# Optimization experiments

Measured on AMD Instinct MI355X. Metric: run time of the kernel, lower is better.

Reference implementation:

```python
import math
import jax, jax.numpy as jnp
import numpy as np

B, L, DM = 2, 1024, 1024
STATE, EXPAND, CONV, DTR = 16, 2, 4, 8
INNER = DM * EXPAND          # 2048
NFFT = L // 2 + 1            # 513


def _silu(v):
    return v * jax.nn.sigmoid(v)


def setup_inputs() -> dict:
    key = jax.random.key(0)
    ks = jax.random.split(key, 12)
    s = lambda k, shape, sc=0.02: (jax.random.normal(k, shape, jnp.float32) * sc)
    # dt_proj bias initialized like the torch module: exp(U(0,1)*(log dt_max - log dt_min) + log dt_min)
    inv_dt = jnp.exp(jax.random.uniform(ks[10], (INNER,), jnp.float32)
                     * (math.log(0.1) - math.log(0.001)) + math.log(0.001))
    return {
        "x": jax.random.normal(ks[0], (B, L, DM), jnp.float32),
        "in_proj_w": s(ks[1], (2 * INNER, DM)),
        "conv_w": s(ks[2], (INNER, 1, CONV), 0.1),      # depthwise conv kernel
        "conv_b": jnp.zeros((INNER,), jnp.float32),
        "A_log": jnp.tile(jnp.log(jnp.arange(1, STATE + 1, dtype=jnp.float32)), (INNER, 1)),
        "D": jnp.ones((INNER,), jnp.float32),
        "x_proj_w": s(ks[3], (DTR + 2 * STATE, INNER)),
        "dt_proj_w": s(ks[4], (INNER, DTR)),
        "dt_proj_b": inv_dt,
        "filter_real": s(ks[5], (INNER, NFFT)),
        "filter_imag": s(ks[6], (INNER, NFFT)),
        "spectral_decay": jnp.ones((INNER,), jnp.float32) * 0.01,
        "fusion_w": s(ks[7], (INNER, 2 * INNER)),
        "fusion_b": jnp.zeros((INNER,), jnp.float32),
        "out_proj_w": s(ks[8], (DM, INNER)),
        "ln_gamma": jnp.ones((DM,), jnp.float32),
        "ln_beta": jnp.zeros((DM,), jnp.float32),
    }


def reference(x, in_proj_w, conv_w, conv_b, A_log, D, x_proj_w, dt_proj_w, dt_proj_b,
              filter_real, filter_imag, spectral_decay, fusion_w, fusion_b,
              out_proj_w, ln_gamma, ln_beta):
    residual = x
    xz = x @ in_proj_w.T                                   # [B,L,2*INNER]
    x_inner, z = xz[..., :INNER], xz[..., INNER:]
    z = _silu(z)

    # ---- SSM path ----
    xc = jnp.swapaxes(x_inner, 1, 2)                       # [B,E,L]
    xc = jax.lax.conv_general_dilated(
        xc, conv_w, (1,), [(CONV - 1, 0)],                 # causal depthwise conv (pad-left == torch pad + truncate)
        dimension_numbers=("NCH", "OIH", "NCH"),
        feature_group_count=INNER) + conv_b[None, :, None]
    x_conv = jnp.swapaxes(_silu(xc), 1, 2)                 # [B,L,E]

    x_dbc = x_conv @ x_proj_w.T                            # [B,L,DTR+2S]
    dt_x = x_dbc[..., :DTR]
    Bm = x_dbc[..., DTR:DTR + STATE]                       # [B,L,S]
    Cm = x_dbc[..., DTR + STATE:]                          # [B,L,S]
    dt = jax.nn.softplus(dt_x @ dt_proj_w.T + dt_proj_b)   # [B,L,E]
    A = -jnp.exp(A_log)                                    # [E,S]
    dA = jnp.exp(dt[..., None] * A)                        # [B,L,E,S]
    dBx = (dt * x_conv)[..., None] * Bm[:, :, None, :]     # [B,L,E,S]

    def step(h, inp):
        dA_t, dBx_t, C_t = inp
        h = dA_t * h + dBx_t                               # [B,E,S]
        return h, jnp.einsum('bes,bs->be', h, C_t)

    h0 = jnp.zeros((B, INNER, STATE), x.dtype)
    _, ys = jax.lax.scan(step, h0,
                         (jnp.swapaxes(dA, 0, 1), jnp.swapaxes(dBx, 0, 1), jnp.swapaxes(Cm, 0, 1)))
    y_ssm = jnp.swapaxes(ys, 0, 1) + x_conv * D            # [B,L,E]

    # ---- Spectral path ----
    xf = jnp.fft.rfft(jnp.swapaxes(x_inner, 1, 2), axis=-1)        # [B,E,NFFT]
    freqs = jnp.linspace(0.0, 1.0, NFFT)
    filt = (filter_real + 1j * filter_imag) * jnp.exp(-spectral_decay[:, None] * freqs[None, :])
    y_spec = jnp.swapaxes(jnp.fft.irfft(xf * filt[None], n=L, axis=-1), 1, 2)  # [B,L,E]

    # ---- Gated fusion ----
    g = jax.nn.sigmoid(jnp.concatenate([y_ssm, y_spec], -1) @ fusion_w.T + fusion_b)
    y = g * y_ssm + (1.0 - g) * y_spec
    y = y * z
    out = y @ out_proj_w.T + residual                      # [B,L,DM]

    mu = out.mean(-1, keepdims=True)
    var = out.var(-1, keepdims=True)
    return (out - mu) / jnp.sqrt(var + 1e-5) * ln_gamma + ln_beta
```

## Files before the change

### kernel.cpp

```cpp
#include <hip/hip_runtime.h>
#include <math.h>

#define B_ 2
#define L_ 1024
#define DM_ 1024
#define STATE_ 16
#define CONV_ 4
#define DTR_ 8
#define INNER_ 2048
#define M_ (B_*L_)
#define MD_ (B_*INNER_)
#define NFFT_ 513
#define NFP_ 1088
#define NCH_ 32
#define CHL_ 32
#define SK_ 16
#define KSL_ (2048/SK_)

typedef unsigned short u16;
typedef __attribute__((ext_vector_type(8))) short short8;
typedef __attribute__((ext_vector_type(8))) __bf16 bf16x8;
typedef __attribute__((ext_vector_type(4))) float f32x4;

__device__ __forceinline__ float frcp_(float x) { return __builtin_amdgcn_rcpf(x); }
__device__ __forceinline__ float fexp_(float x) { return __expf(x); }
__device__ __forceinline__ float fsigm_(float x) { return frcp_(1.f + __expf(-x)); }
__device__ __forceinline__ float fsilu_(float x) { return x * frcp_(1.f + __expf(-x)); }
__device__ __forceinline__ float fsoftplus_(float v) {
  return (v > 20.f) ? v : __logf(1.f + __expf(v));
}
__device__ __forceinline__ u16 f2bf(float f) {
  union { float f; unsigned u; } v; v.f = f;
  unsigned r = v.u + 0x7fffu + ((v.u >> 16) & 1u);
  return (u16)(r >> 16);
}
__device__ __forceinline__ float bf2f(u16 h) {
  union { unsigned u; float f; } v; v.u = ((unsigned)h) << 16;
  return v.f;
}
__device__ __forceinline__ void gload16(const void* g, void* l) {
  __builtin_amdgcn_global_load_lds(
      (const __attribute__((address_space(1))) unsigned*)g,
      (__attribute__((address_space(3))) unsigned*)l, 16, 0, 0);
}
__device__ __forceinline__ f32x4 mfma_bf16(short8 a, short8 b, f32x4 c) {
  return __builtin_amdgcn_mfma_f32_16x16x32_bf16(
      __builtin_bit_cast(bf16x8, a), __builtin_bit_cast(bf16x8, b), c, 0, 0, 0);
}

#define CVT2_N0 2097152
#define CVT2_NT 6291456
__global__ __launch_bounds__(256) void cvt2_k(
    const float* __restrict__ s0, const float* __restrict__ s1,
    u16* __restrict__ out)
{
  int i = (blockIdx.x*256 + threadIdx.x) * 4;
  const float* src; int off;
  if (i < CVT2_N0) { src = s0; off = 0; }
  else             { src = s1; off = CVT2_N0; }
  float4 v = *(const float4*)(src + (i - off));
  ushort4 o;
  o.x = f2bf(v.x); o.y = f2bf(v.y); o.z = f2bf(v.z); o.w = f2bf(v.w);
  *(ushort4*)(out + i) = o;
}

__device__ __forceinline__ void cvt16_body(int eb, int nthr, int t,
    const float* __restrict__ src, u16* __restrict__ dst)
{
  int i = (eb*nthr + t)*16;
  #pragma unroll
  for (int q = 0; q < 4; q++) {
    float4 v = *(const float4*)(src + i + q*4);
    ushort4 o;
    o.x = f2bf(v.x); o.y = f2bf(v.y); o.z = f2bf(v.z); o.w = f2bf(v.w);
    *(ushort4*)(dst + i + q*4) = o;
  }
}

__device__ __forceinline__ void conv_body(int idx, const float* __restrict__ xz,
    const float* __restrict__ cw, const float* __restrict__ cb,
    float* __restrict__ xc)
{
  int c = idx & (INNER_-1);
  int g = idx >> 11;
  int b = g >> 7;
  int lb = (g & 127) * 8;
  float w0=cw[c*4+0], w1=cw[c*4+1], w2=cw[c*4+2], w3=cw[c*4+3];
  float bias = cb[c];
  float v[11];
  #pragma unroll
  for (int j = 0; j < 11; j++) {
    int l = lb - 3 + j;
    v[j] = (l >= 0) ? xz[((size_t)((b << 10) + l))*4096 + c] : 0.f;
  }
  #pragma unroll
  for (int j = 0; j < 8; j++) {
    float s = bias + w0*v[j] + w1*v[j+1] + w2*v[j+2] + w3*v[j+3];
    xc[((size_t)((b << 10) + lb + j))*INNER_ + c] = fsilu_(s);
  }
}

__device__ __forceinline__ void genWdft_body(int idx, u16* __restrict__ W)
{
  int l = idx & (L_-1);
  int col = idx >> 10;
  float v = 0.f;
  int f = col >> 1;
  if (f < NFFT_) {
    int ph = (l*f) & (L_-1);
    float th = (float)ph * (6.283185307179586f / (float)L_);
    v = (col & 1) ? -__sinf(th) : __cosf(th);
  }
  W[idx] = f2bf(v);
}

__device__ __forceinline__ void genWinv_body(int idx, u16* __restrict__ W)
{
  int r = idx % NFP_;
  int l = idx / NFP_;
  int f = r >> 1;
  float v = 0.f;
  if (f < NFFT_) {
    bool edge = (f == 0) || (f == 512);
    float sc = (edge ? 1.f : 2.f) / (float)L_;
    int ph = (f*l) & (L_-1);
    float th = (float)ph * (6.283185307179586f / (float)L_);
    if (r & 1) v = edge ? 0.f : -sc*__sinf(th);
    else       v = sc*__cosf(th);
  }
  W[idx] = f2bf(v);
}

__device__ __forceinline__ void xproj_body(int eb,
    const float* __restrict__ xconv, const float* __restrict__ W,
    float* __restrict__ part, void* lds)
{
  float (*Bs)[KSL_+4] = (float(*)[KSL_+4])lds;
  const int sk = eb & (SK_-1), mt = eb / SK_;
  const int k0 = sk*KSL_;
  for (int i = threadIdx.x; i < 40*KSL_; i += 256) {
    int n = i / KSL_, k = i & (KSL_-1);
    Bs[n][k] = W[(size_t)n*2048 + k0 + k];
  }
  __syncthreads();
  const int m = mt*256 + threadIdx.x;
  const float* arow = xconv + (size_t)m*2048 + k0;
  float acc[40];
  #pragma unroll
  for (int j=0;j<40;j++) acc[j]=0.f;
  for (int k = 0; k < KSL_; k += 4) {
    float4 a = *(const float4*)(arow + k);
    #pragma unroll
    for (int j = 0; j < 40; j++) {
      float4 b = *(const float4*)&Bs[j][k];
      acc[j] += a.x*b.x + a.y*b.y + a.z*b.z + a.w*b.w;
    }
  }
  float* o = part + ((size_t)sk*M_ + m)*40;
  #pragma unroll
  for (int j = 0; j < 10; j++)
    *(float4*)(o + j*4) = make_float4(acc[j*4], acc[j*4+1], acc[j*4+2], acc[j*4+3]);
}

template<int TM, int TN, int EPI, int YCH, int AUX, int KS>
__global__ __launch_bounds__((TM/64)*(TN/32)*64) void mgemm_k(
    const u16* __restrict__ Ab, const u16* __restrict__ Bb,
    void* __restrict__ Cout, int K, int ldc,
    const float* __restrict__ aux0, u16* __restrict__ aux1,
    const float* __restrict__ aux2, const float* __restrict__ aux3,
    int gx, int gy,
    const float* __restrict__ ga, const float* __restrict__ gb,
    const float* __restrict__ gc, float* __restrict__ go,
    u16* __restrict__ gw,
    int ldk, const float* __restrict__ cvs, u16* __restrict__ cvd)
{
  constexpr int WN   = TN/32;
  constexpr int NW   = (TM/64)*WN;
  constexpr int NTHR = NW*64;
  __shared__ __align__(16) u16 As[2][TM*64];
  __shared__ __align__(16) u16 Bs[2][TN*64];
  const int t = threadIdx.x;
  const int nwg = gx * gy;

  if constexpr (AUX != 0) {
    int eb = (int)blockIdx.x - nwg*KS;
    if (eb >= 0) {
      if constexpr (AUX == 1) {
        if (eb < 2176) genWdft_body(eb*NTHR + t, gw);
        else           cvt16_body(eb - 2176, NTHR, t, cvs, cvd);
      } else if constexpr (AUX == 2) {
        if (eb < 2048)      conv_body(eb*256 + t, ga, gb, gc, go);
        else if (eb < 6400) genWinv_body((eb - 2048)*256 + t, gw);
        else                cvt16_body(eb - 6400, NTHR, t, cvs, cvd);
      } else {
        xproj_body(eb, ga, gb, go, (void*)&As[0][0]);
      }
      return;
    }
  }

  const int lane = t & 63;
  const int w = t >> 6;
  const int wm = w / WN, wn = w % WN;

  int bid = blockIdx.x;
  int ks = 0;
  if constexpr (KS > 1) { ks = bid / nwg; bid -= ks*nwg; }
  const int k0 = ks * K;
  const int lid = (bid & 7) * (nwg >> 3) + (bid >> 3);
  int bx, by;
  if (YCH) { by = lid / gx; bx = lid - by*gx; }
  else     { bx = lid / gy; by = lid - bx*gy; }
  const int M0 = by * TM, N0 = bx * TN;

  f32x4 acc[4][2] = {};

  auto stage = [&](int buf, int kk0) {
    #pragma unroll
    for (int q = 0; q < TM*8/NTHR; q++) {
      int u = q*NTHR + t;
      int row = u >> 3, gpr = u & 7;
      int grp = gpr ^ (row & 7);
      gload16(Ab + (size_t)(M0+row)*ldk + k0 + kk0 + grp*8, &As[buf][u*8]);
    }
    #pragma unroll
    for (int q = 0; q < TN*8/NTHR; q++) {
      int u = q*NTHR + t;
      int row = u >> 3, gpr = u & 7;
      int grp = gpr ^ (row & 7);
      gload16(Bb + (size_t)(N0+row)*ldk + k0 + kk0 + grp*8, &Bs[buf][u*8]);
    }
  };

  stage(0, 0);
  const int nk = K >> 6;
  for (int kst = 0; kst < nk; kst++) {
    const int buf = kst & 1;
    __syncthreads();
    if (kst + 1 < nk) stage(buf ^ 1, (kst + 1) << 6);
    const u16* Asb = As[buf];
    const u16* Bsb = Bs[buf];
    #pragma unroll
    for (int kk = 0; kk < 2; kk++) {
      const int quad = lane >> 4;
      const int grp = kk*4 + quad;
      short8 af[4], bfr[2];
      #pragma unroll
      for (int i = 0; i < 4; i++) {
        int row = wm*64 + i*16 + (lane & 15);
        af[i] = *(const short8*)&Asb[(row*8 + (grp ^ (row & 7)))*8];
      }
      #pragma unroll
      for (int j = 0; j < 2; j++) {
        int row = wn*32 + j*16 + (lane & 15);
        bfr[j] = *(const short8*)&Bsb[(row*8 + (grp ^ (row & 7)))*8];
      }
      #pragma unroll
      for (int i = 0; i < 4; i++)
        #pragma unroll
        for (int j = 0; j < 2; j++)
          acc[i][j] = mfma_bf16(af[i], bfr[j], acc[i][j]);
    }
  }

  #pragma unroll
  for (int i = 0; i < 4; i++) {
    int mbase = M0 + wm*64 + i*16 + (lane >> 4)*4;
    #pragma unroll
    for (int j = 0; j < 2; j++) {
      int n = N0 + wn*32 + j*16 + (lane & 15);
      #pragma unroll
      for (int r = 0; r < 4; r++) {
        int m = mbase + r;
        float v = acc[i][j][r];
        if (EPI == 0) {
          ((float*)Cout)[(size_t)m*ldc + n] = v;
        } else if (EPI == 3) {
          float pv = __shfl_xor(v, 1, 64);
          int f = n >> 1;
          float outv = 0.f;
          if (f < NFFT_) {
            int c = m & (INNER_-1);
            float d  = fexp_(-aux2[c] * (float)f * (1.f/512.f));
            float wr = aux0[c*NFFT_+f]*d, wi = aux3[c*NFFT_+f]*d;
            float a = (n & 1) ? pv : v;
            float b = (n & 1) ? v : pv;
            outv = (n & 1) ? (a*wi + b*wr) : (a*wr - b*wi);
          }
          ((u16*)Cout)[(size_t)m*ldc + n] = f2bf(outv);
        } else if (EPI == 5) {
          ((float*)Cout)[(size_t)m*ldc + n] = v;
          if (n < 2048) {
            int b2 = m >> 10, l2 = m & 1023;
            aux1[((size_t)(b2*2048 + n) << 10) + l2] = f2bf(v);
          }
        } else if (EPI == 6) {
          int b2 = m >> 11, c2 = m & (INNER_-1);
          ((u16*)Cout)[((size_t)((b2 << 10) + n) << 12) + 2048 + c2] = f2bf(v);
        } else {
          float* P = (float*)Cout + (size_t)ks * ((size_t)gy*TM*ldc);
          P[(size_t)m*ldc + n] = v;
        }
      }
    }
  }
}

__global__ __launch_bounds__(256) void combine_gate_k(
    const float* __restrict__ P, const float* __restrict__ fus_b,
    const u16* __restrict__ ycat, const float* __restrict__ xz,
    u16* __restrict__ ycomb)
{
  int i4 = (blockIdx.x*256 + threadIdx.x)*4;
  int m = i4 >> 11, n = i4 & 2047;
  float4 p0 = *(const float4*)(P + i4);
  float4 p1 = *(const float4*)(P + 4194304 + i4);
  ushort4 ysv = *(const ushort4*)(ycat + (size_t)m*4096 + n);
  ushort4 ypv = *(const ushort4*)(ycat + (size_t)m*4096 + 2048 + n);
  float4 zv = *(const float4*)(xz + (size_t)m*4096 + 2048 + n);
  float4 fb = *(const float4*)(fus_b + n);
  float pp[4] = {p0.x+p1.x, p0.y+p1.y, p0.z+p1.z, p0.w+p1.w};
  float zz[4] = {zv.x, zv.y, zv.z, zv.w};
  float bb[4] = {fb.x, fb.y, fb.z, fb.w};
  u16 ys[4] = {ysv.x, ysv.y, ysv.z, ysv.w};
  u16 yp[4] = {ypv.x, ypv.y, ypv.z, ypv.w};
  ushort4 o;
  u16* op = (u16*)&o;
  #pragma unroll
  for (int j = 0; j < 4; j++) {
    float g = fsigm_(pp[j] + bb[j]);
    op[j] = f2bf((g*bf2f(ys[j]) + (1.f-g)*bf2f(yp[j]))*fsilu_(zz[j]));
  }
  *(ushort4*)(ycomb + i4) = o;
}

__global__ __launch_bounds__(256) void xpred_k(const float* __restrict__ part,
                                               float* __restrict__ xdbc)
{
  int i = blockIdx.x*256 + threadIdx.x;
  float s = 0.f;
  #pragma unroll
  for (int sk = 0; sk < SK_; sk++) s += part[(size_t)sk*81920 + i];
  xdbc[i] = s;
}

__global__ __launch_bounds__(256) void scan1_k(
    const float* __restrict__ xdbc, const float* __restrict__ xconv,
    const float* __restrict__ A_log, const float* __restrict__ dtw,
    const float* __restrict__ dtb, float* __restrict__ Pq)
{
  int idx = blockIdx.x*256 + threadIdx.x;
  int e  = idx & (INNER_-1);
  int bc = idx >> 11;
  int ch = bc & (NCH_-1);
  int b  = bc >> 5;
  float A[STATE_];
  #pragma unroll
  for (int s=0;s<STATE_;s++) A[s] = -fexp_(A_log[e*STATE_+s]);
  float w[DTR_];
  #pragma unroll
  for (int r=0;r<DTR_;r++) w[r] = dtw[e*DTR_+r];
  float bias = dtb[e];
  float h[STATE_] = {};
  float sdt = 0.f;
  int mbase = b*L_ + ch*CHL_;
  float dtx[DTR_], Bv[STATE_], xcv;
  {
    const float* row = xdbc + (size_t)mbase*40;
    #pragma unroll
    for (int r=0;r<DTR_;r++) dtx[r] = row[r];
    #pragma unroll
    for (int s=0;s<STATE_;s++) Bv[s] = row[8+s];
    xcv = xconv[(size_t)mbase*INNER_ + e];
  }
  for (int l=0;l<CHL_;l++) {
    float ndtx[DTR_], nBv[STATE_], nxcv = 0.f;
    if (l+1 < CHL_) {
      const float* nrow = xdbc + (size_t)(mbase+l+1)*40;
      #pragma unroll
      for (int r=0;r<DTR_;r++) ndtx[r] = nrow[r];
      #pragma unroll
      for (int s=0;s<STATE_;s++) nBv[s] = nrow[8+s];
      nxcv = xconv[(size_t)(mbase+l+1)*INNER_ + e];
    } else {
      #pragma unroll
      for (int r=0;r<DTR_;r++) ndtx[r] = 0.f;
      #pragma unroll
      for (int s=0;s<STATE_;s++) nBv[s] = 0.f;
    }
    float v = bias;
    #pragma unroll
    for (int r=0;r<DTR_;r++) v += dtx[r]*w[r];
    float dt = fsoftplus_(v);
    sdt += dt;
    float dx = dt * xcv;
    #pragma unroll
    for (int s=0;s<STATE_;s++) {
      float dA = fexp_(dt*A[s]);
      h[s] = dA*h[s] + dx*Bv[s];
    }
    #pragma unroll
    for (int r=0;r<DTR_;r++) dtx[r] = ndtx[r];
    #pragma unroll
    for (int s=0;s<STATE_;s++) Bv[s] = nBv[s];
    xcv = nxcv;
  }
  float* o = Pq + (size_t)idx*32;
  #pragma unroll
  for (int s=0;s<STATE_;s++) { o[s] = fexp_(A[s]*sdt); o[16+s] = h[s]; }
}

__global__ __launch_bounds__(256) void scan2_k(float* __restrict__ Pq)
{
  int idx = blockIdx.x*256 + threadIdx.x;
  int s = idx & 15;
  int e = (idx >> 4) & (INNER_-1);
  int b = idx >> 15;
  float h = 0.f;
  for (int ch = 0; ch < NCH_; ch++) {
    size_t base = ((size_t)(b*NCH_+ch)*INNER_ + e)*32;
    float p = Pq[base + s];
    float q = Pq[base + 16 + s];
    Pq[base + 16 + s] = h;
    h = p*h + q;
  }
}

__global__ __launch_bounds__(256) void scan3_k(
    const float* __restrict__ xdbc, const float* __restrict__ xconv,
    const float* __restrict__ A_log, const float* __restrict__ dtw,
    const float* __restrict__ dtb, const float* __restrict__ Dp,
    const float* __restrict__ Pq, u16* __restrict__ ycat)
{
  int idx = blockIdx.x*256 + threadIdx.x;
  int e  = idx & (INNER_-1);
  int bc = idx >> 11;
  int ch = bc & (NCH_-1);
  int b  = bc >> 5;
  float A[STATE_];
  #pragma unroll
  for (int s=0;s<STATE_;s++) A[s] = -fexp_(A_log[e*STATE_+s]);
  float w[DTR_];
  #pragma unroll
  for (int r=0;r<DTR_;r++) w[r] = dtw[e*DTR_+r];
  float bias = dtb[e];
  float Dv = Dp[e];
  float h[STATE_];
  const float* hi = Pq + (size_t)idx*32 + 16;
  #pragma unroll
  for (int s=0;s<STATE_;s++) h[s] = hi[s];
  int mbase = b*L_ + ch*CHL_;
  float dtx[DTR_], Bv[STATE_], Cv[STATE_], xcv;
  {
    const float* row = xdbc + (size_t)mbase*40;
    #pragma unroll
    for (int r=0;r<DTR_;r++) dtx[r] = row[r];
    #pragma unroll
    for (int s=0;s<STATE_;s++) { Bv[s] = row[8+s]; Cv[s] = row[24+s]; }
    xcv = xconv[(size_t)mbase*INNER_ + e];
  }
  for (int l=0;l<CHL_;l++) {
    float ndtx[DTR_], nBv[STATE_], nCv[STATE_], nxcv = 0.f;
    if (l+1 < CHL_) {
      const float* nrow = xdbc + (size_t)(mbase+l+1)*40;
      #pragma unroll
      for (int r=0;r<DTR_;r++) ndtx[r] = nrow[r];
      #pragma unroll
      for (int s=0;s<STATE_;s++) { nBv[s] = nrow[8+s]; nCv[s] = nrow[24+s]; }
      nxcv = xconv[(size_t)(mbase+l+1)*INNER_ + e];
    } else {
      #pragma unroll
      for (int r=0;r<DTR_;r++) ndtx[r] = 0.f;
      #pragma unroll
      for (int s=0;s<STATE_;s++) { nBv[s] = 0.f; nCv[s] = 0.f; }
    }
    float v = bias;
    #pragma unroll
    for (int r=0;r<DTR_;r++) v += dtx[r]*w[r];
    float dt = fsoftplus_(v);
    float dx = dt * xcv;
    float y = 0.f;
    #pragma unroll
    for (int s=0;s<STATE_;s++) {
      float dA = fexp_(dt*A[s]);
      h[s] = dA*h[s] + dx*Bv[s];
      y += h[s]*Cv[s];
    }
    ycat[(size_t)(mbase+l)*4096 + e] = f2bf(y + xcv*Dv);
    #pragma unroll
    for (int r=0;r<DTR_;r++) dtx[r] = ndtx[r];
    #pragma unroll
    for (int s=0;s<STATE_;s++) { Bv[s] = nBv[s]; Cv[s] = nCv[s]; }
    xcv = nxcv;
  }
}

__global__ __launch_bounds__(256) void ln2_k(const float* __restrict__ Q,
    const float* __restrict__ xres,
    const float* __restrict__ gma, const float* __restrict__ bta,
    float* __restrict__ out)
{
  int m = blockIdx.x;
  float s=0.f, s2=0.f;
  float v[4];
  #pragma unroll
  for (int j=0;j<4;j++) {
    int n = threadIdx.x + j*256;
    size_t idx = (size_t)m*DM_ + n;
    v[j] = Q[idx] + Q[2097152 + idx] + xres[idx];
    s += v[j]; s2 += v[j]*v[j];
  }
  #pragma unroll
  for (int off=32; off>=1; off>>=1) {
    s  += __shfl_down(s, off);
    s2 += __shfl_down(s2, off);
  }
  __shared__ float rs[4], rs2[4], stats[2];
  int wid = threadIdx.x >> 6;
  if ((threadIdx.x & 63) == 0) { rs[wid]=s; rs2[wid]=s2; }
  __syncthreads();
  if (threadIdx.x == 0) {
    float ts  = rs[0]+rs[1]+rs[2]+rs[3];
    float ts2 = rs2[0]+rs2[1]+rs2[2]+rs2[3];
    float mu  = ts/(float)DM_;
    float var = ts2/(float)DM_ - mu*mu;
    stats[0] = mu; stats[1] = rsqrtf(var + 1e-5f);
  }
  __syncthreads();
  float mu = stats[0], rstd = stats[1];
  #pragma unroll
  for (int j=0;j<4;j++) {
    int n = threadIdx.x + j*256;
    out[(size_t)m*DM_ + n] = (v[j]-mu)*rstd*gma[n] + bta[n];
  }
}

extern "C" void kernel_launch(void* const* d_in, const int* in_sizes, int n_in,
                              void* d_out, int out_size, void* d_ws, size_t ws_size,
                              hipStream_t stream)
{
  const float* x       = (const float*)d_in[0];
  const float* in_w    = (const float*)d_in[1];
  const float* conv_w  = (const float*)d_in[2];
  const float* conv_b  = (const float*)d_in[3];
  const float* A_log   = (const float*)d_in[4];
  const float* Dp      = (const float*)d_in[5];
  const float* xproj_w = (const float*)d_in[6];
  const float* dt_w    = (const float*)d_in[7];
  const float* dt_b    = (const float*)d_in[8];
  const float* f_re    = (const float*)d_in[9];
  const float* f_im    = (const float*)d_in[10];
  const float* s_dec   = (const float*)d_in[11];
  const float* fus_w   = (const float*)d_in[12];
  const float* fus_b   = (const float*)d_in[13];
  const float* out_w   = (const float*)d_in[14];
  const float* ln_g    = (const float*)d_in[15];
  const float* ln_b    = (const float*)d_in[16];
  float* out = (float*)d_out;

  float* ws    = (float*)d_ws;
  float* xz    = ws;
  float* xconv = xz    + 8388608;
  float* xdbc  = xconv + 4194304;
  float* Pq    = xdbc  + 81920;
  u16* ub      = (u16*)(Pq + 4194304);
  u16* xb      = ub;
  u16* inwb    = xb    + 2097152;
  u16* fuswb   = inwb  + 4194304;
  u16* outwb   = fuswb + 8388608;
  u16* xt      = outwb + 2097152;
  u16* Wb      = xt    + 4194304;
  u16* XFb     = Wb    + 1114112;
  u16* ycat    = XFb   + 4456448;
  u16* ycomb   = xt;
  u16* Winv    = xb;
  float* part  = (float*)inwb;
  float* fpart = xconv;
  float* opart = Pq;

  cvt2_k<<<CVT2_NT/1024, 256, 0, stream>>>(x, in_w, xb);

  mgemm_k<128,128,5,0,1,1><<<512 + 2176 + 1024, 512, 0, stream>>>(
      xb, inwb, xz, 1024, 4096, nullptr, xt, nullptr, nullptr, 32, 16,
      nullptr, nullptr, nullptr, nullptr, Wb, 1024, fus_w, fuswb);
  mgemm_k<128,64,3,1,2,1><<<544 + 2048 + 4352 + 512, 256, 0, stream>>>(
      xt, Wb, XFb, 1024, NFP_, f_re, nullptr, s_dec, f_im, 17, 32,
      xz, conv_w, conv_b, xconv, Winv, 1024, out_w, outwb);
  mgemm_k<128,64,6,1,3,1><<<512 + SK_*8, 256, 0, stream>>>(
      XFb, Winv, ycat, NFP_, 0, nullptr, nullptr, nullptr, nullptr, 16, 32,
      xconv, xproj_w, nullptr, part, nullptr, NFP_, nullptr, nullptr);
  xpred_k<<<(M_*40)/256, 256, 0, stream>>>(part, xdbc);
  scan1_k<<<(B_*NCH_*INNER_)/256, 256, 0, stream>>>(xdbc, xconv, A_log, dt_w, dt_b, Pq);
  scan2_k<<<(B_*INNER_*STATE_)/256, 256, 0, stream>>>(Pq);
  scan3_k<<<(B_*NCH_*INNER_)/256, 256, 0, stream>>>(xdbc, xconv, A_log, dt_w, dt_b, Dp, Pq, ycat);
  mgemm_k<128,128,7,0,0,2><<<2*256, 512, 0, stream>>>(
      ycat, fuswb, fpart, 2048, 2048, nullptr, nullptr, nullptr, nullptr, 16, 16,
      nullptr, nullptr, nullptr, nullptr, nullptr, 4096, nullptr, nullptr);
  combine_gate_k<<<(2048*2048/4)/256, 256, 0, stream>>>(
      fpart, fus_b, ycat, xz, ycomb);
  mgemm_k<64,64,7,1,0,2><<<2*512, 128, 0, stream>>>(
      ycomb, outwb, opart, 1024, 1024, nullptr, nullptr, nullptr, nullptr, 16, 32,
      nullptr, nullptr, nullptr, nullptr, nullptr, 2048, nullptr, nullptr);
  ln2_k<<<M_, 256, 0, stream>>>(opart, x, ln_g, ln_b, out);
}
```

Before: 395.5 us.

## Restructure aux work placement, transpose inverse-DFT epilogue via LDS, bf16 fusion partials

The first GEMM's epilogue no longer writes the transposed bf16 copy of x_inner. Instead a new standalone aux kernel (conv, Winv generation, out_w conversion) produces that copy from the fp32 result during the conv pass. The xproj side-work moves into the forward-DFT GEMM, and the split-K reduction (xpred) folds into the inverse-DFT GEMM launch, removing one kernel launch. The inverse-DFT epilogue now transposes through LDS so it issues coalesced 16-byte stores instead of strided scalar u16 writes. The fusion-GEMM split-K partials are stored as bf16 to halve traffic, at some cost in precision.

Result: faster. 369.9 us (-6.5%).

```diff
diff --git a/kernel.cpp b/kernel.cpp
--- a/kernel.cpp
+++ b/kernel.cpp
@@ -77,9 +77,9 @@
   }
 }
 
-__device__ __forceinline__ void conv_body(int idx, const float* __restrict__ xz,
+__device__ __forceinline__ void conv_xt_body(int idx, const float* __restrict__ xz,
     const float* __restrict__ cw, const float* __restrict__ cb,
-    float* __restrict__ xc)
+    float* __restrict__ xc, u16* __restrict__ xt)
 {
   int c = idx & (INNER_-1);
   int g = idx >> 11;
@@ -93,6 +93,10 @@
     int l = lb - 3 + j;
     v[j] = (l >= 0) ? xz[((size_t)((b << 10) + l))*4096 + c] : 0.f;
   }
+  union { u16 a[8]; short8 v8; } tu;
+  #pragma unroll
+  for (int j = 0; j < 8; j++) tu.a[j] = f2bf(v[j+3]);
+  *(short8*)&xt[(((size_t)(b*INNER_ + c)) << 10) + lb] = tu.v8;
   #pragma unroll
   for (int j = 0; j < 8; j++) {
     float s = bias + w0*v[j] + w1*v[j+1] + w2*v[j+2] + w3*v[j+3];
@@ -162,6 +166,27 @@
     *(float4*)(o + j*4) = make_float4(acc[j*4], acc[j*4+1], acc[j*4+2], acc[j*4+3]);
 }
 
+__device__ __forceinline__ void xpred_body(int i, const float* __restrict__ part,
+                                           float* __restrict__ xdbc)
+{
+  float s = 0.f;
+  #pragma unroll
+  for (int sk = 0; sk < SK_; sk++) s += part[(size_t)sk*81920 + i];
+  xdbc[i] = s;
+}
+
+__global__ __launch_bounds__(256) void aux2_k(
+    const float* __restrict__ xz, const float* __restrict__ cw,
+    const float* __restrict__ cb, float* __restrict__ xc,
+    u16* __restrict__ xt, u16* __restrict__ Winv,
+    const float* __restrict__ ows, u16* __restrict__ owd)
+{
+  int eb = blockIdx.x;
+  if (eb < 2048)      conv_xt_body(eb*256 + threadIdx.x, xz, cw, cb, xc, xt);
+  else if (eb < 6400) genWinv_body((eb - 2048)*256 + threadIdx.x, Winv);
+  else                cvt16_body(eb - 6400, 256, threadIdx.x, ows, owd);
+}
+
 template<int TM, int TN, int EPI, int YCH, int AUX, int KS>
 __global__ __launch_bounds__((TM/64)*(TN/32)*64) void mgemm_k(
     const u16* __restrict__ Ab, const u16* __restrict__ Bb,
@@ -170,8 +195,7 @@
     const float* __restrict__ aux2, const float* __restrict__ aux3,
     int gx, int gy,
     const float* __restrict__ ga, const float* __restrict__ gb,
-    const float* __restrict__ gc, float* __restrict__ go,
-    u16* __restrict__ gw,
+    float* __restrict__ go, u16* __restrict__ gw,
     int ldk, const float* __restrict__ cvs, u16* __restrict__ cvd)
 {
   constexpr int WN   = TN/32;
@@ -188,12 +212,10 @@
       if constexpr (AUX == 1) {
         if (eb < 2176) genWdft_body(eb*NTHR + t, gw);
         else           cvt16_body(eb - 2176, NTHR, t, cvs, cvd);
-      } else if constexpr (AUX == 2) {
-        if (eb < 2048)      conv_body(eb*256 + t, ga, gb, gc, go);
-        else if (eb < 6400) genWinv_body((eb - 2048)*256 + t, gw);
-        else                cvt16_body(eb - 6400, NTHR, t, cvs, cvd);
+      } else if constexpr (AUX == 3) {
+        xproj_body(eb, ga, gb, go, (void*)&As[0][0]);
       } else {
-        xproj_body(eb, ga, gb, go, (void*)&As[0][0]);
+        xpred_body(eb*256 + t, ga, go);
       }
       return;
     }
@@ -263,43 +285,65 @@
     }
   }
 
-  #pragma unroll
-  for (int i = 0; i < 4; i++) {
-    int mbase = M0 + wm*64 + i*16 + (lane >> 4)*4;
-    #pragma unroll
-    for (int j = 0; j < 2; j++) {
-      int n = N0 + wn*32 + j*16 + (lane & 15);
-      #pragma unroll
-      for (int r = 0; r < 4; r++) {
-        int m = mbase + r;
-        float v = acc[i][j][r];
-        if (EPI == 0) {
-          ((float*)Cout)[(size_t)m*ldc + n] = v;
-        } else if (EPI == 3) {
-          float pv = __shfl_xor(v, 1, 64);
-          int f = n >> 1;
-          float outv = 0.f;
-          if (f < NFFT_) {
-            int c = m & (INNER_-1);
-            float d  = fexp_(-aux2[c] * (float)f * (1.f/512.f));
-            float wr = aux0[c*NFFT_+f]*d, wi = aux3[c*NFFT_+f]*d;
-            float a = (n & 1) ? pv : v;
-            float b = (n & 1) ? v : pv;
-            outv = (n & 1) ? (a*wi + b*wr) : (a*wr - b*wi);
+  if constexpr (EPI == 6) {
+    u16* T = (u16*)&As[0][0];
+    __syncthreads();
+    #pragma unroll
+    for (int i = 0; i < 4; i++) {
+      int cb = wm*64 + i*16 + (lane >> 4)*4;
+      #pragma unroll
+      for (int j = 0; j < 2; j++) {
+        int ll = wn*32 + j*16 + (lane & 15);
+        #pragma unroll
+        for (int r = 0; r < 4; r++)
+          T[(cb + r)*66 + ll] = f2bf(acc[i][j][r]);
+      }
+    }
+    __syncthreads();
+    const int b2 = M0 >> 11, c0 = M0 & (INNER_-1);
+    u16* yc = (u16*)Cout;
+    #pragma unroll
+    for (int q = 0; q < (TM*TN/8)/NTHR; q++) {
+      int task = q*NTHR + t;
+      int cg = task & 15, ll = task >> 4;
+      union { u16 a[8]; short8 v8; } tu;
+      #pragma unroll
+      for (int e = 0; e < 8; e++) tu.a[e] = T[(cg*8 + e)*66 + ll];
+      *(short8*)&yc[((size_t)((b2 << 10) + N0 + ll) << 12) + 2048 + c0 + cg*8] = tu.v8;
+    }
+  } else {
+    #pragma unroll
+    for (int i = 0; i < 4; i++) {
+      int mbase = M0 + wm*64 + i*16 + (lane >> 4)*4;
+      #pragma unroll
+      for (int j = 0; j < 2; j++) {
+        int n = N0 + wn*32 + j*16 + (lane & 15);
+        #pragma unroll
+        for (int r = 0; r < 4; r++) {
+          int m = mbase + r;
+          float v = acc[i][j][r];
+          if (EPI == 0) {
+            ((float*)Cout)[(size_t)m*ldc + n] = v;
+          } else if (EPI == 3) {
+            float pv = __shfl_xor(v, 1, 64);
+            int f = n >> 1;
+            float outv = 0.f;
+            if (f < NFFT_) {
+              int c = m & (INNER_-1);
+              float d  = fexp_(-aux2[c] * (float)f * (1.f/512.f));
+              float wr = aux0[c*NFFT_+f]*d, wi = aux3[c*NFFT_+f]*d;
+              float a = (n & 1) ? pv : v;
+              float b = (n & 1) ? v : pv;
+              outv = (n & 1) ? (a*wi + b*wr) : (a*wr - b*wi);
+            }
+            ((u16*)Cout)[(size_t)m*ldc + n] = f2bf(outv);
+          } else if (EPI == 7) {
+            float* P = (float*)Cout + (size_t)ks * ((size_t)gy*TM*ldc);
+            P[(size_t)m*ldc + n] = v;
+          } else {
+            u16* P = (u16*)Cout + (size_t)ks * ((size_t)gy*TM*ldc);
+            P[(size_t)m*ldc + n] = f2bf(v);
           }
-          ((u16*)Cout)[(size_t)m*ldc + n] = f2bf(outv);
-        } else if (EPI == 5) {
-          ((float*)Cout)[(size_t)m*ldc + n] = v;
-          if (n < 2048) {
-            int b2 = m >> 10, l2 = m & 1023;
-            aux1[((size_t)(b2*2048 + n) << 10) + l2] = f2bf(v);
-          }
-        } else if (EPI == 6) {
-          int b2 = m >> 11, c2 = m & (INNER_-1);
-          ((u16*)Cout)[((size_t)((b2 << 10) + n) << 12) + 2048 + c2] = f2bf(v);
-        } else {
-          float* P = (float*)Cout + (size_t)ks * ((size_t)gy*TM*ldc);
-          P[(size_t)m*ldc + n] = v;
         }
       }
     }
@@ -307,19 +351,20 @@
 }
 
 __global__ __launch_bounds__(256) void combine_gate_k(
-    const float* __restrict__ P, const float* __restrict__ fus_b,
+    const u16* __restrict__ P, const float* __restrict__ fus_b,
     const u16* __restrict__ ycat, const float* __restrict__ xz,
     u16* __restrict__ ycomb)
 {
   int i4 = (blockIdx.x*256 + threadIdx.x)*4;
   int m = i4 >> 11, n = i4 & 2047;
-  float4 p0 = *(const float4*)(P + i4);
-  float4 p1 = *(const float4*)(P + 4194304 + i4);
+  ushort4 p0 = *(const ushort4*)(P + i4);
+  ushort4 p1 = *(const ushort4*)(P + 4194304 + i4);
   ushort4 ysv = *(const ushort4*)(ycat + (size_t)m*4096 + n);
   ushort4 ypv = *(const ushort4*)(ycat + (size_t)m*4096 + 2048 + n);
   float4 zv = *(const float4*)(xz + (size_t)m*4096 + 2048 + n);
   float4 fb = *(const float4*)(fus_b + n);
-  float pp[4] = {p0.x+p1.x, p0.y+p1.y, p0.z+p1.z, p0.w+p1.w};
+  float pp[4] = {bf2f(p0.x)+bf2f(p1.x), bf2f(p0.y)+bf2f(p1.y),
+                 bf2f(p0.z)+bf2f(p1.z), bf2f(p0.w)+bf2f(p1.w)};
   float zz[4] = {zv.x, zv.y, zv.z, zv.w};
   float bb[4] = {fb.x, fb.y, fb.z, fb.w};
   u16 ys[4] = {ysv.x, ysv.y, ysv.z, ysv.w};
@@ -332,16 +377,6 @@
     op[j] = f2bf((g*bf2f(ys[j]) + (1.f-g)*bf2f(yp[j]))*fsilu_(zz[j]));
   }
   *(ushort4*)(ycomb + i4) = o;
-}
-
-__global__ __launch_bounds__(256) void xpred_k(const float* __restrict__ part,
-                                               float* __restrict__ xdbc)
-{
-  int i = blockIdx.x*256 + threadIdx.x;
-  float s = 0.f;
-  #pragma unroll
-  for (int sk = 0; sk < SK_; sk++) s += part[(size_t)sk*81920 + i];
-  xdbc[i] = s;
 }
 
 __global__ __launch_bounds__(256) void scan1_k(
@@ -575,31 +610,31 @@
   u16* ycomb   = xt;
   u16* Winv    = xb;
   float* part  = (float*)inwb;
-  float* fpart = xconv;
+  u16* fpart   = (u16*)xconv;
   float* opart = Pq;
 
   cvt2_k<<<CVT2_NT/1024, 256, 0, stream>>>(x, in_w, xb);
 
-  mgemm_k<128,128,5,0,1,1><<<512 + 2176 + 1024, 512, 0, stream>>>(
-      xb, inwb, xz, 1024, 4096, nullptr, xt, nullptr, nullptr, 32, 16,
-      nullptr, nullptr, nullptr, nullptr, Wb, 1024, fus_w, fuswb);
-  mgemm_k<128,64,3,1,2,1><<<544 + 2048 + 4352 + 512, 256, 0, stream>>>(
+  mgemm_k<128,128,0,0,1,1><<<512 + 2176 + 1024, 512, 0, stream>>>(
+      xb, inwb, xz, 1024, 4096, nullptr, nullptr, nullptr, nullptr, 32, 16,
+      nullptr, nullptr, nullptr, Wb, 1024, fus_w, fuswb);
+  aux2_k<<<6912, 256, 0, stream>>>(xz, conv_w, conv_b, xconv, xt, Winv, out_w, outwb);
+  mgemm_k<128,64,3,1,3,1><<<544 + SK_*8, 256, 0, stream>>>(
       xt, Wb, XFb, 1024, NFP_, f_re, nullptr, s_dec, f_im, 17, 32,
-      xz, conv_w, conv_b, xconv, Winv, 1024, out_w, outwb);
-  mgemm_k<128,64,6,1,3,1><<<512 + SK_*8, 256, 0, stream>>>(
+      xconv, xproj_w, part, nullptr, 1024, nullptr, nullptr);
+  mgemm_k<128,64,6,1,4,1><<<512 + 320, 256, 0, stream>>>(
       XFb, Winv, ycat, NFP_, 0, nullptr, nullptr, nullptr, nullptr, 16, 32,
-      xconv, xproj_w, nullptr, part, nullptr, NFP_, nullptr, nullptr);
-  xpred_k<<<(M_*40)/256, 256, 0, stream>>>(part, xdbc);
+      part, nullptr, xdbc, nullptr, NFP_, nullptr, nullptr);
   scan1_k<<<(B_*NCH_*INNER_)/256, 256, 0, stream>>>(xdbc, xconv, A_log, dt_w, dt_b, Pq);
   scan2_k<<<(B_*INNER_*STATE_)/256, 256, 0, stream>>>(Pq);
   scan3_k<<<(B_*NCH_*INNER_)/256, 256, 0, stream>>>(xdbc, xconv, A_log, dt_w, dt_b, Dp, Pq, ycat);
-  mgemm_k<128,128,7,0,0,2><<<2*256, 512, 0, stream>>>(
+  mgemm_k<128,128,8,0,0,2><<<2*256, 512, 0, stream>>>(
       ycat, fuswb, fpart, 2048, 2048, nullptr, nullptr, nullptr, nullptr, 16, 16,
-      nullptr, nullptr, nullptr, nullptr, nullptr, 4096, nullptr, nullptr);
+      nullptr, nullptr, nullptr, nullptr, 4096, nullptr, nullptr);
   combine_gate_k<<<(2048*2048/4)/256, 256, 0, stream>>>(
       fpart, fus_b, ycat, xz, ycomb);
   mgemm_k<64,64,7,1,0,2><<<2*512, 128, 0, stream>>>(
       ycomb, outwb, opart, 1024, 1024, nullptr, nullptr, nullptr, nullptr, 16, 32,
-      nullptr, nullptr, nullptr, nullptr, nullptr, 2048, nullptr, nullptr);
+      nullptr, nullptr, nullptr, nullptr, 2048, nullptr, nullptr);
   ln2_k<<<M_, 256, 0, stream>>>(opart, x, ln_g, ln_b, out);
 }
```
